# Optimization experiments

Hardware: AMD Instinct MI355X
Metric: run time of the kernel (lower is better)

Reference implementation:

```python
import jax, jax.numpy as jnp
import numpy as np

N_NODES = 100000
N_EDGES = 2000000
F_IN = 32
HID = 32
N_CLASS = 40


def _gru_cell(m, h, wih, whh, bih, bhh):
    # torch.nn.GRUCell math; wih/whh: [3H, H_in], gates ordered r, z, n
    gi = m @ wih.T + bih
    gh = h @ whh.T + bhh
    i_r, i_z, i_n = jnp.split(gi, 3, axis=-1)
    h_r, h_z, h_n = jnp.split(gh, 3, axis=-1)
    r = jax.nn.sigmoid(i_r + h_r)
    z = jax.nn.sigmoid(i_z + h_z)
    n = jnp.tanh(i_n + r * h_n)
    return (1.0 - z) * n + z * h


def _gated_conv(x, edge_index, edge_weight, w_proj, w_msg, wih, whh, bih, bhh):
    h = x @ w_proj                                   # [N, out]
    msg = (h @ w_msg)[edge_index[0]] * edge_weight[:, None]  # gather src -> [E, out]
    agg = jax.ops.segment_sum(msg, edge_index[1], num_segments=N_NODES)  # scatter-add to dst
    return _gru_cell(agg, h, wih, whh, bih, bhh)


def setup_inputs() -> dict:
    key = jax.random.key(0)
    ks = jax.random.split(key, 16)
    s = 0.1
    return {
        "x": jax.random.normal(ks[0], (N_NODES, F_IN), jnp.float32),
        "edge_index": jax.random.randint(ks[1], (2, N_EDGES), 0, N_NODES, jnp.int64),
        "edge_weight": jax.random.uniform(ks[2], (N_EDGES,), jnp.float32),
        "W1_proj": jax.random.normal(ks[3], (F_IN, HID), jnp.float32) * s,
        "W1_msg": jax.random.normal(ks[4], (HID, HID), jnp.float32) * s,
        "gru1_wih": jax.random.normal(ks[5], (3 * HID, HID), jnp.float32) * s,
        "gru1_whh": jax.random.normal(ks[6], (3 * HID, HID), jnp.float32) * s,
        "gru1_bih": jax.random.normal(ks[7], (3 * HID,), jnp.float32) * s,
        "gru1_bhh": jax.random.normal(ks[8], (3 * HID,), jnp.float32) * s,
        "W2_proj": jax.random.normal(ks[9], (HID, N_CLASS), jnp.float32) * s,
        "W2_msg": jax.random.normal(ks[10], (N_CLASS, N_CLASS), jnp.float32) * s,
        "gru2_wih": jax.random.normal(ks[11], (3 * N_CLASS, N_CLASS), jnp.float32) * s,
        "gru2_whh": jax.random.normal(ks[12], (3 * N_CLASS, N_CLASS), jnp.float32) * s,
        "gru2_bih": jax.random.normal(ks[13], (3 * N_CLASS,), jnp.float32) * s,
        "gru2_bhh": jax.random.normal(ks[14], (3 * N_CLASS,), jnp.float32) * s,
    }


def reference(x, edge_index, edge_weight, W1_proj, W1_msg, gru1_wih, gru1_whh,
              gru1_bih, gru1_bhh, W2_proj, W2_msg, gru2_wih, gru2_whh,
              gru2_bih, gru2_bhh):
    # eval mode: dropout is identity
    h = _gated_conv(x, edge_index, edge_weight, W1_proj, W1_msg,
                    gru1_wih, gru1_whh, gru1_bih, gru1_bhh)
    h = jax.nn.relu(h)
    h = _gated_conv(h, edge_index, edge_weight, W2_proj, W2_msg,
                    gru2_wih, gru2_whh, gru2_bih, gru2_bhh)
    return jax.nn.log_softmax(h, axis=-1)
```

## Files before the change

### kernel.cpp

```cpp
#include <hip/hip_runtime.h>
#include <math.h>

#define NN 100000
#define NP 100032
#define NE 2000000
#define FIN 32
#define H 32
#define NC 40

#define NBK 196
#define BSH 9
#define CAP 10880
#define EPT 16
#define EPB (256 * EPT)

typedef _Float16 half_t;
typedef __attribute__((ext_vector_type(8))) _Float16 half8;
typedef __attribute__((ext_vector_type(4))) _Float16 half4;
typedef __attribute__((ext_vector_type(4))) float f32x4;
typedef long long ll2 __attribute__((ext_vector_type(2)));

__device__ __forceinline__ float sigm_(float x) {
    return 1.0f / (1.0f + __expf(-x));
}
__device__ __forceinline__ float tanh_(float x) {
    x = fminf(fmaxf(x, -20.0f), 20.0f);
    float e = __expf(2.0f * x);
    return (e - 1.0f) / (e + 1.0f);
}

__global__ __launch_bounds__(256) void kA_bucket(const int* __restrict__ ei,
                                                 const float* __restrict__ ew,
                                                 int* __restrict__ gcur,
                                                 long long* __restrict__ rec) {
    __shared__ long long recs[EPB];
    __shared__ int gdst[EPB];
    __shared__ int cnt[NBK], base[NBK], sofs[NBK];
    __shared__ int ssc[256];
    int tid = threadIdx.x;
    for (int i = tid; i < NBK; i += 256) cnt[i] = 0;
    __syncthreads();
    int e0 = blockIdx.x * EPB;
    int dcache[EPT];
#pragma unroll
    for (int i = 0; i < EPT; ++i) {
        int e = e0 + i * 256 + tid;
        dcache[i] = (e < NE) ? ei[NE + e] : -1;
        if (e < NE) atomicAdd(&cnt[dcache[i] >> BSH], 1);
    }
    __syncthreads();
    int cv = (tid < NBK) ? cnt[tid] : 0;
    ssc[tid] = cv;
    __syncthreads();
    for (int off = 1; off < 256; off <<= 1) {
        int v = (tid >= off) ? ssc[tid - off] : 0;
        __syncthreads();
        ssc[tid] += v;
        __syncthreads();
    }
    if (tid < NBK) {
        sofs[tid] = ssc[tid] - cv;
        base[tid] = atomicAdd(&gcur[tid], cv);
        cnt[tid] = 0;
    }
    __syncthreads();
#pragma unroll
    for (int i = 0; i < EPT; ++i) {
        int e = e0 + i * 256 + tid;
        if (e < NE) {
            int d = dcache[i], s = ei[e];
            int b = d >> BSH;
            int r = atomicAdd(&cnt[b], 1);
            int slot = sofs[b] + r;
            int pos = base[b] + r;
            int lo = s | ((d & 511) << 17);
            recs[slot] = (long long)(unsigned)lo |
                         ((long long)__float_as_int(ew[e]) << 32);
            gdst[slot] = (pos < CAP) ? (b * CAP + pos) : -1;
        }
    }
    __syncthreads();
    int nrec = min(EPB, NE - e0);
    for (int i = tid; i < nrec; i += 256) {
        int gd = gdst[i];
        if (gd >= 0) rec[gd] = recs[i];
    }
}

__global__ __launch_bounds__(256) void kB_sort(const int* __restrict__ gcur,
                                               const int2* __restrict__ rec,
                                               int2* __restrict__ evs,
                                               int* __restrict__ ofs,
                                               int* __restrict__ ocn) {
    __shared__ int hist[2048], lofs[2048], ssc[256];
    int tid = threadIdx.x, b = blockIdx.x;
    int nb0 = b << BSH;
    int nnodes = min(512, NN - nb0);
    int cntb = min(gcur[b], CAP);
    for (int i = tid; i < 2048; i += 256) hist[i] = 0;
    __syncthreads();
    const int2* rb = rec + (size_t)b * CAP;
    for (int i = tid; i < cntb; i += 256) {
        int rx = rb[i].x;
        int bin = (((rx >> 17) & 511) << 2) | ((rx & 0x1FFFF) >> 15);
        atomicAdd(&hist[bin], 1);
    }
    __syncthreads();
    int base = tid * 8, ls = 0, lh[8];
#pragma unroll
    for (int j = 0; j < 8; ++j) {
        lh[j] = hist[base + j];
        ls += lh[j];
    }
    ssc[tid] = ls;
    __syncthreads();
    for (int off = 1; off < 256; off <<= 1) {
        int v = (tid >= off) ? ssc[tid - off] : 0;
        __syncthreads();
        ssc[tid] += v;
        __syncthreads();
    }
    int ex = ssc[tid] - ls;
#pragma unroll
    for (int j = 0; j < 8; ++j) {
        lofs[base + j] = ex;
        ex += lh[j];
    }
    __syncthreads();
    for (int l = tid; l < nnodes; l += 256) {
        int c = hist[4 * l] + hist[4 * l + 1] + hist[4 * l + 2] + hist[4 * l + 3];
        ofs[nb0 + l] = b * CAP + lofs[4 * l];
        ocn[nb0 + l] = c;
    }
    __syncthreads();
    for (int i = tid; i < 2048; i += 256) hist[i] = 0;
    __syncthreads();
    int2* eb = evs + (size_t)b * CAP;
    for (int i = tid; i < cntb; i += 256) {
        int2 r = rb[i];
        int bin = (((r.x >> 17) & 511) << 2) | ((r.x & 0x1FFFF) >> 15);
        int rk = atomicAdd(&hist[bin], 1);
        eb[lofs[bin] + rk] = make_int2(r.x & 0x1FFFF, r.y);
    }
}

__global__ __launch_bounds__(256) void k_wpre(const float* __restrict__ W2m,
                                              const float* __restrict__ wih2,
                                              float* __restrict__ M2,
                                              int* __restrict__ gcur) {
    int i = blockIdx.x * 256 + threadIdx.x;
    if (i < NBK) gcur[i] = 0;
    if (i >= NC * 3 * NC) return;
    int u = i / (3 * NC), col = i % (3 * NC);
    float acc = 0.f;
#pragma unroll
    for (int t = 0; t < NC; ++t) acc += W2m[u * NC + t] * wih2[col * NC + t];
    M2[i] = acc;
}

__global__ __launch_bounds__(256) void k_wc(const float* __restrict__ W1m,
                                            const float* __restrict__ wih1,
                                            const float* __restrict__ W2p,
                                            const float* __restrict__ M2,
                                            const float* __restrict__ whh1,
                                            const float* __restrict__ whh2,
                                            half_t* __restrict__ W1sw,
                                            half_t* __restrict__ W2sw) {
    int i = blockIdx.x * 256 + threadIdx.x;
    if (i < 8192) {
        int j = i & 7, lane = (i >> 3) & 63, ct = (i >> 9) & 7, s = i >> 12;
        int k = s * 32 + (lane >> 4) * 8 + j;
        int col = ct * 16 + (lane & 15);
        int g = col >> 5, jj = col & 31;
        float v = 0.f;
        if (g <= 2) {
            if (k < 32) {
                float acc = 0.f;
#pragma unroll
                for (int t = 0; t < H; ++t) acc += W1m[k * H + t] * wih1[(g * H + jj) * H + t];
                v = acc;
            } else if (g < 2) {
                v = whh1[(g * H + jj) * H + (k - 32)];
            }
        } else {
            if (k >= 32) v = whh1[(2 * H + jj) * H + (k - 32)];
        }
        W1sw[i] = (half_t)v;
    } else if (i < 8192 + 18432) {
        int i2 = i - 8192;
        int j = i2 & 7, lane = (i2 >> 3) & 63;
        int tt = i2 >> 9;
        int ct = tt % 12, s = tt / 12;
        int k = s * 32 + (lane >> 4) * 8 + j;
        int col = ct * 16 + (lane & 15);
        int g = col / 48, jj = col % 48;
        float v = 0.f;
        if (jj < NC) {
            if (g <= 2) {
                if (k < 32) {
                    float acc = 0.f;
#pragma unroll
                    for (int u = 0; u < NC; ++u)
                        acc += W2p[k * NC + u] * M2[u * 3 * NC + g * NC + jj];
                    v = acc;
                } else if (k < 72 && g < 2) {
                    v = whh2[(g * NC + jj) * NC + (k - 32)];
                }
            } else {
                if (k >= 32 && k < 72) v = whh2[(2 * NC + jj) * NC + (k - 32)];
            }
        }
        W2sw[i2] = (half_t)v;
    }
}

__global__ __launch_bounds__(256) void k1_proj(const float* __restrict__ x,
                                               const float* __restrict__ Wp,
                                               half_t* __restrict__ Xc1,
                                               half_t* __restrict__ Hd) {
    __shared__ float sWp[FIN * H];
    __shared__ float sx[8][FIN];
    int tid = threadIdx.x;
    for (int i = tid; i < FIN * H; i += 256) sWp[i] = Wp[i];
    int nb = blockIdx.x * 8;
    int nl = tid >> 5, j = tid & 31;
    int n = nb + nl;
    if (n < NN) sx[nl][j] = x[(size_t)n * FIN + j];
    __syncthreads();
    float acc = 0.f;
#pragma unroll
    for (int k = 0; k < FIN; ++k) acc += sx[nl][k] * sWp[k * H + j];
    if (n < NN) {
        half_t hv = (half_t)acc;
        Xc1[(size_t)n * 64 + 32 + j] = hv;
        Hd[(size_t)n * 32 + j] = hv;
    }
}

__global__ __launch_bounds__(320) void k4_proj2(const half_t* __restrict__ Hh,
                                                const float* __restrict__ Wp,
                                                half_t* __restrict__ Xc2) {
    __shared__ float sWp[FIN * NC];
    __shared__ float shn[8][FIN];
    int tid = threadIdx.x;
    for (int i = tid; i < FIN * NC; i += 320) sWp[i] = Wp[i];
    int nb = blockIdx.x * 8;
    if (tid < 256) {
        int r = tid >> 5, c = tid & 31;
        shn[r][c] = (float)Hh[(size_t)(nb + r) * 32 + c];
    }
    if (tid < 192) {
        int r = tid / 24, c = tid % 24;
        Xc2[(size_t)(nb + r) * 96 + 72 + c] = (half_t)0.f;
    }
    __syncthreads();
    int nl = tid / NC, j = tid % NC;
    int n = nb + nl;
    float acc = 0.f;
#pragma unroll
    for (int k = 0; k < FIN; ++k) acc += shn[nl][k] * sWp[k * NC + j];
    if (n < NN) Xc2[(size_t)n * 96 + 32 + j] = (half_t)acc;
}

template <int DSTR>
__global__ __launch_bounds__(256) void k_aggh(const int* __restrict__ ofs,
                                              const int* __restrict__ ocn,
                                              const int2* __restrict__ evs,
                                              const half_t* __restrict__ src,
                                              half_t* __restrict__ dst) {
    int idx = blockIdx.x * 256 + threadIdx.x;
    int n = idx >> 2, q = idx & 3;
    if (n >= NN) return;
    const half8* s8 = (const half8*)src + q;
    const long long* ev8 = (const long long*)evs;
    int e = ofs[n];
    int e1 = e + ocn[n];
    float acc[8] = {0.f, 0.f, 0.f, 0.f, 0.f, 0.f, 0.f, 0.f};
    if ((e & 1) && e < e1) {
        long long r = __builtin_nontemporal_load(ev8 + e);
        float w = __int_as_float((int)(r >> 32));
        half8 hv = s8[(size_t)(r & 0x1FFFF) * 4];
#pragma unroll
        for (int t = 0; t < 8; ++t) acc[t] += w * (float)hv[t];
        ++e;
    }
    for (; e + 8 <= e1; e += 8) {
        ll2 p0 = __builtin_nontemporal_load((const ll2*)(ev8 + e));
        ll2 p1 = __builtin_nontemporal_load((const ll2*)(ev8 + e + 2));
        ll2 p2 = __builtin_nontemporal_load((const ll2*)(ev8 + e + 4));
        ll2 p3 = __builtin_nontemporal_load((const ll2*)(ev8 + e + 6));
        half8 h0 = s8[(size_t)(p0[0] & 0x1FFFF) * 4];
        half8 h1 = s8[(size_t)(p0[1] & 0x1FFFF) * 4];
        half8 h2 = s8[(size_t)(p1[0] & 0x1FFFF) * 4];
        half8 h3 = s8[(size_t)(p1[1] & 0x1FFFF) * 4];
        half8 h4 = s8[(size_t)(p2[0] & 0x1FFFF) * 4];
        half8 h5 = s8[(size_t)(p2[1] & 0x1FFFF) * 4];
        half8 h6 = s8[(size_t)(p3[0] & 0x1FFFF) * 4];
        half8 h7 = s8[(size_t)(p3[1] & 0x1FFFF) * 4];
        float w0 = __int_as_float((int)(p0[0] >> 32));
        float w1 = __int_as_float((int)(p0[1] >> 32));
        float w2 = __int_as_float((int)(p1[0] >> 32));
        float w3 = __int_as_float((int)(p1[1] >> 32));
        float w4 = __int_as_float((int)(p2[0] >> 32));
        float w5 = __int_as_float((int)(p2[1] >> 32));
        float w6 = __int_as_float((int)(p3[0] >> 32));
        float w7 = __int_as_float((int)(p3[1] >> 32));
#pragma unroll
        for (int t = 0; t < 8; ++t) {
            acc[t] += w0 * (float)h0[t];
            acc[t] += w1 * (float)h1[t];
            acc[t] += w2 * (float)h2[t];
            acc[t] += w3 * (float)h3[t];
            acc[t] += w4 * (float)h4[t];
            acc[t] += w5 * (float)h5[t];
            acc[t] += w6 * (float)h6[t];
            acc[t] += w7 * (float)h7[t];
        }
    }
    if (e + 4 <= e1) {
        ll2 p0 = __builtin_nontemporal_load((const ll2*)(ev8 + e));
        ll2 p1 = __builtin_nontemporal_load((const ll2*)(ev8 + e + 2));
        half8 h0 = s8[(size_t)(p0[0] & 0x1FFFF) * 4];
        half8 h1 = s8[(size_t)(p0[1] & 0x1FFFF) * 4];
        half8 h2 = s8[(size_t)(p1[0] & 0x1FFFF) * 4];
        half8 h3 = s8[(size_t)(p1[1] & 0x1FFFF) * 4];
        float w0 = __int_as_float((int)(p0[0] >> 32));
        float w1 = __int_as_float((int)(p0[1] >> 32));
        float w2 = __int_as_float((int)(p1[0] >> 32));
        float w3 = __int_as_float((int)(p1[1] >> 32));
#pragma unroll
        for (int t = 0; t < 8; ++t) {
            acc[t] += w0 * (float)h0[t];
            acc[t] += w1 * (float)h1[t];
            acc[t] += w2 * (float)h2[t];
            acc[t] += w3 * (float)h3[t];
        }
        e += 4;
    }
    if (e + 2 <= e1) {
        ll2 p0 = __builtin_nontemporal_load((const ll2*)(ev8 + e));
        half8 h0 = s8[(size_t)(p0[0] & 0x1FFFF) * 4];
        half8 h1 = s8[(size_t)(p0[1] & 0x1FFFF) * 4];
        float w0 = __int_as_float((int)(p0[0] >> 32));
        float w1 = __int_as_float((int)(p0[1] >> 32));
#pragma unroll
        for (int t = 0; t < 8; ++t) {
            acc[t] += w0 * (float)h0[t];
            acc[t] += w1 * (float)h1[t];
        }
        e += 2;
    }
    if (e < e1) {
        long long r = __builtin_nontemporal_load(ev8 + e);
        float w = __int_as_float((int)(r >> 32));
        half8 hv = s8[(size_t)(r & 0x1FFFF) * 4];
#pragma unroll
        for (int t = 0; t < 8; ++t) acc[t] += w * (float)hv[t];
    }
    half8 o;
#pragma unroll
    for (int t = 0; t < 8; ++t) o[t] = (half_t)acc[t];
    *(half8*)(dst + (size_t)n * DSTR + q * 8) = o;
}

__global__ __launch_bounds__(256) void k3m(const half_t* __restrict__ Xc1,
                                           const half8* __restrict__ W1sw,
                                           const float* __restrict__ bih,
                                           const float* __restrict__ bhh,
                                           half_t* __restrict__ Hh) {
    int tid = threadIdx.x;
    int wave = tid >> 6, lane = tid & 63;
    int m16 = lane & 15, q = lane >> 4;
    int nb = blockIdx.x * 64 + wave * 16;
    const half8* xr = (const half8*)(Xc1 + (size_t)(nb + m16) * 64);
    half8 a0 = xr[q];
    half8 a1 = xr[4 + q];
    f32x4 acc[8];
#pragma unroll
    for (int ct = 0; ct < 8; ++ct) acc[ct] = (f32x4){0.f, 0.f, 0.f, 0.f};
#pragma unroll
    for (int ct = 0; ct < 8; ++ct) {
        acc[ct] = __builtin_amdgcn_mfma_f32_16x16x32_f16(a0, W1sw[ct * 64 + lane], acc[ct], 0, 0, 0);
        acc[ct] = __builtin_amdgcn_mfma_f32_16x16x32_f16(a1, W1sw[(8 + ct) * 64 + lane], acc[ct], 0, 0, 0);
    }
#pragma unroll
    for (int ct = 0; ct < 2; ++ct) {
        int j = ct * 16 + m16;
        float br = bih[j] + bhh[j];
        float bz = bih[H + j] + bhh[H + j];
        float bi = bih[2 * H + j], bh = bhh[2 * H + j];
#pragma unroll
        for (int m = 0; m < 4; ++m) {
            int node = nb + q * 4 + m;
            float r = sigm_(acc[ct][m] + br);
            float z = sigm_(acc[2 + ct][m] + bz);
            float ng = tanh_(acc[4 + ct][m] + bi + r * (acc[6 + ct][m] + bh));
            float hj = (float)Xc1[(size_t)node * 64 + 32 + j];
            float o = fmaxf((1.f - z) * ng + z * hj, 0.f);
            if (node < NN) Hh[(size_t)node * 32 + j] = (half_t)o;
        }
    }
}

__global__ __launch_bounds__(256) void k6m(const half_t* __restrict__ Xc2,
                                           const half8* __restrict__ W2sw,
                                           const float* __restrict__ bih,
                                           const float* __restrict__ bhh,
                                           float* __restrict__ out) {
    int tid = threadIdx.x;
    int wave = tid >> 6, lane = tid & 63;
    int m16 = lane & 15, q = lane >> 4;
    int nb = blockIdx.x * 64 + wave * 16;
    const half8* xr = (const half8*)(Xc2 + (size_t)(nb + m16) * 96);
    half8 a0 = xr[q], a1 = xr[4 + q], a2 = xr[8 + q];
    f32x4 acc[12];
#pragma unroll
    for (int ct = 0; ct < 12; ++ct) acc[ct] = (f32x4){0.f, 0.f, 0.f, 0.f};
#pragma unroll
    for (int ct = 0; ct < 12; ++ct) {
        acc[ct] = __builtin_amdgcn_mfma_f32_16x16x32_f16(a0, W2sw[ct * 64 + lane], acc[ct], 0, 0, 0);
        acc[ct] = __builtin_amdgcn_mfma_f32_16x16x32_f16(a1, W2sw[(12 + ct) * 64 + lane], acc[ct], 0, 0, 0);
        acc[ct] = __builtin_amdgcn_mfma_f32_16x16x32_f16(a2, W2sw[(24 + ct) * 64 + lane], acc[ct], 0, 0, 0);
    }
    float v[3][4];
#pragma unroll
    for (int ct = 0; ct < 3; ++ct) {
        int j = ct * 16 + m16;
        int jc = (j < NC) ? j : (NC - 1);
        float br = bih[jc] + bhh[jc];
        float bz = bih[NC + jc] + bhh[NC + jc];
        float bi = bih[2 * NC + jc], bh = bhh[2 * NC + jc];
#pragma unroll
        for (int m = 0; m < 4; ++m) {
            int node = nb + q * 4 + m;
            float r = sigm_(acc[ct][m] + br);
            float z = sigm_(acc[3 + ct][m] + bz);
            float ng = tanh_(acc[6 + ct][m] + bi + r * (acc[9 + ct][m] + bh));
            float hj = (float)Xc2[(size_t)node * 96 + 32 + jc];
            v[ct][m] = (1.f - z) * ng + z * hj;
        }
    }
    bool v2ok = (m16 < 8);
#pragma unroll
    for (int m = 0; m < 4; ++m) {
        float mx = fmaxf(v[0][m], v[1][m]);
        if (v2ok) mx = fmaxf(mx, v[2][m]);
#pragma unroll
        for (int d = 1; d < 16; d <<= 1) mx = fmaxf(mx, __shfl_xor(mx, d));
        float se = __expf(v[0][m] - mx) + __expf(v[1][m] - mx) +
                   (v2ok ? __expf(v[2][m] - mx) : 0.f);
#pragma unroll
        for (int d = 1; d < 16; d <<= 1) se += __shfl_xor(se, d);
        float ls = mx + __logf(se);
        int node = nb + q * 4 + m;
        if (node < NN) {
            out[(size_t)node * NC + m16] = v[0][m] - ls;
            out[(size_t)node * NC + 16 + m16] = v[1][m] - ls;
            if (v2ok) out[(size_t)node * NC + 32 + m16] = v[2][m] - ls;
        }
    }
}

extern "C" void kernel_launch(void* const* d_in, const int* in_sizes, int n_in,
                              void* d_out, int out_size, void* d_ws, size_t ws_size,
                              hipStream_t stream) {
    const float* x = (const float*)d_in[0];
    const int* ei = (const int*)d_in[1];
    const float* ew = (const float*)d_in[2];
    const float* W1p = (const float*)d_in[3];
    const float* W1m = (const float*)d_in[4];
    const float* g1wih = (const float*)d_in[5];
    const float* g1whh = (const float*)d_in[6];
    const float* g1bih = (const float*)d_in[7];
    const float* g1bhh = (const float*)d_in[8];
    const float* W2p = (const float*)d_in[9];
    const float* W2m = (const float*)d_in[10];
    const float* g2wih = (const float*)d_in[11];
    const float* g2whh = (const float*)d_in[12];
    const float* g2bih = (const float*)d_in[13];
    const float* g2bhh = (const float*)d_in[14];
    float* ws = (float*)d_ws;

    half_t* Xc = (half_t*)ws;
    half_t* Hd = (half_t*)(ws + 3201024);
    half_t* Hh = (half_t*)(ws + 4801536);
    int2* rec = (int2*)ws;
    int2* evs = (int2*)(ws + 6402048);
    int* ofs = (int*)(ws + 10667008);
    int* ocn = (int*)(ws + 10767008);
    int* gcur = (int*)(ws + 10867008);
    half_t* W1sw = (half_t*)(ws + 10867264);
    half_t* W2sw = W1sw + 8192;
    float* M2 = ws + 10880576;
    float* out = (float*)d_out;

    k_wpre<<<(NC * 3 * NC + 255) / 256, 256, 0, stream>>>(W2m, g2wih, M2, gcur);
    kA_bucket<<<(NE + EPB - 1) / EPB, 256, 0, stream>>>(ei, ew, gcur, (long long*)rec);
    kB_sort<<<NBK, 256, 0, stream>>>(gcur, rec, evs, ofs, ocn);
    k_wc<<<(8192 + 18432 + 255) / 256, 256, 0, stream>>>(
        W1m, g1wih, W2p, M2, g1whh, g2whh, W1sw, W2sw);

    k1_proj<<<NN / 8, 256, 0, stream>>>(x, W1p, Xc, Hd);
    k_aggh<64><<<(NN * 4 + 255) / 256, 256, 0, stream>>>(ofs, ocn, evs, Hd, Xc);
    k3m<<<NP / 64, 256, 0, stream>>>(Xc, (const half8*)W1sw, g1bih, g1bhh, Hh);

    k4_proj2<<<NN / 8, 320, 0, stream>>>(Hh, W2p, Xc);
    k_aggh<96><<<(NN * 4 + 255) / 256, 256, 0, stream>>>(ofs, ocn, evs, Hh, Xc);
    k6m<<<NP / 64, 256, 0, stream>>>(Xc, (const half8*)W2sw, g2bih, g2bhh, out);
}
```

Before: 303.7 us.

## Fuse aggregation, projection and GRU per layer into single kernels

```diff
diff --git a/kernel.cpp b/kernel.cpp
--- a/kernel.cpp
+++ b/kernel.cpp
@@ -14,9 +14,11 @@
 #define EPT 16
 #define EPB (256 * EPT)
 
+#define NPROJ 12500
+#define NWB 104
+
 typedef _Float16 half_t;
 typedef __attribute__((ext_vector_type(8))) _Float16 half8;
-typedef __attribute__((ext_vector_type(4))) _Float16 half4;
 typedef __attribute__((ext_vector_type(4))) float f32x4;
 typedef long long ll2 __attribute__((ext_vector_type(2)));
 
@@ -29,253 +31,16 @@
     return (e - 1.0f) / (e + 1.0f);
 }
 
-__global__ __launch_bounds__(256) void kA_bucket(const int* __restrict__ ei,
-                                                 const float* __restrict__ ew,
-                                                 int* __restrict__ gcur,
-                                                 long long* __restrict__ rec) {
-    __shared__ long long recs[EPB];
-    __shared__ int gdst[EPB];
-    __shared__ int cnt[NBK], base[NBK], sofs[NBK];
-    __shared__ int ssc[256];
-    int tid = threadIdx.x;
-    for (int i = tid; i < NBK; i += 256) cnt[i] = 0;
-    __syncthreads();
-    int e0 = blockIdx.x * EPB;
-    int dcache[EPT];
-#pragma unroll
-    for (int i = 0; i < EPT; ++i) {
-        int e = e0 + i * 256 + tid;
-        dcache[i] = (e < NE) ? ei[NE + e] : -1;
-        if (e < NE) atomicAdd(&cnt[dcache[i] >> BSH], 1);
-    }
-    __syncthreads();
-    int cv = (tid < NBK) ? cnt[tid] : 0;
-    ssc[tid] = cv;
-    __syncthreads();
-    for (int off = 1; off < 256; off <<= 1) {
-        int v = (tid >= off) ? ssc[tid - off] : 0;
-        __syncthreads();
-        ssc[tid] += v;
-        __syncthreads();
-    }
-    if (tid < NBK) {
-        sofs[tid] = ssc[tid] - cv;
-        base[tid] = atomicAdd(&gcur[tid], cv);
-        cnt[tid] = 0;
-    }
-    __syncthreads();
-#pragma unroll
-    for (int i = 0; i < EPT; ++i) {
-        int e = e0 + i * 256 + tid;
-        if (e < NE) {
-            int d = dcache[i], s = ei[e];
-            int b = d >> BSH;
-            int r = atomicAdd(&cnt[b], 1);
-            int slot = sofs[b] + r;
-            int pos = base[b] + r;
-            int lo = s | ((d & 511) << 17);
-            recs[slot] = (long long)(unsigned)lo |
-                         ((long long)__float_as_int(ew[e]) << 32);
-            gdst[slot] = (pos < CAP) ? (b * CAP + pos) : -1;
-        }
-    }
-    __syncthreads();
-    int nrec = min(EPB, NE - e0);
-    for (int i = tid; i < nrec; i += 256) {
-        int gd = gdst[i];
-        if (gd >= 0) rec[gd] = recs[i];
-    }
-}
-
-__global__ __launch_bounds__(256) void kB_sort(const int* __restrict__ gcur,
-                                               const int2* __restrict__ rec,
-                                               int2* __restrict__ evs,
-                                               int* __restrict__ ofs,
-                                               int* __restrict__ ocn) {
-    __shared__ int hist[2048], lofs[2048], ssc[256];
-    int tid = threadIdx.x, b = blockIdx.x;
-    int nb0 = b << BSH;
-    int nnodes = min(512, NN - nb0);
-    int cntb = min(gcur[b], CAP);
-    for (int i = tid; i < 2048; i += 256) hist[i] = 0;
-    __syncthreads();
-    const int2* rb = rec + (size_t)b * CAP;
-    for (int i = tid; i < cntb; i += 256) {
-        int rx = rb[i].x;
-        int bin = (((rx >> 17) & 511) << 2) | ((rx & 0x1FFFF) >> 15);
-        atomicAdd(&hist[bin], 1);
-    }
-    __syncthreads();
-    int base = tid * 8, ls = 0, lh[8];
-#pragma unroll
-    for (int j = 0; j < 8; ++j) {
-        lh[j] = hist[base + j];
-        ls += lh[j];
-    }
-    ssc[tid] = ls;
-    __syncthreads();
-    for (int off = 1; off < 256; off <<= 1) {
-        int v = (tid >= off) ? ssc[tid - off] : 0;
-        __syncthreads();
-        ssc[tid] += v;
-        __syncthreads();
-    }
-    int ex = ssc[tid] - ls;
-#pragma unroll
-    for (int j = 0; j < 8; ++j) {
-        lofs[base + j] = ex;
-        ex += lh[j];
-    }
-    __syncthreads();
-    for (int l = tid; l < nnodes; l += 256) {
-        int c = hist[4 * l] + hist[4 * l + 1] + hist[4 * l + 2] + hist[4 * l + 3];
-        ofs[nb0 + l] = b * CAP + lofs[4 * l];
-        ocn[nb0 + l] = c;
-    }
-    __syncthreads();
-    for (int i = tid; i < 2048; i += 256) hist[i] = 0;
-    __syncthreads();
-    int2* eb = evs + (size_t)b * CAP;
-    for (int i = tid; i < cntb; i += 256) {
-        int2 r = rb[i];
-        int bin = (((r.x >> 17) & 511) << 2) | ((r.x & 0x1FFFF) >> 15);
-        int rk = atomicAdd(&hist[bin], 1);
-        eb[lofs[bin] + rk] = make_int2(r.x & 0x1FFFF, r.y);
-    }
-}
-
-__global__ __launch_bounds__(256) void k_wpre(const float* __restrict__ W2m,
-                                              const float* __restrict__ wih2,
-                                              float* __restrict__ M2,
-                                              int* __restrict__ gcur) {
-    int i = blockIdx.x * 256 + threadIdx.x;
-    if (i < NBK) gcur[i] = 0;
-    if (i >= NC * 3 * NC) return;
-    int u = i / (3 * NC), col = i % (3 * NC);
-    float acc = 0.f;
-#pragma unroll
-    for (int t = 0; t < NC; ++t) acc += W2m[u * NC + t] * wih2[col * NC + t];
-    M2[i] = acc;
-}
-
-__global__ __launch_bounds__(256) void k_wc(const float* __restrict__ W1m,
-                                            const float* __restrict__ wih1,
-                                            const float* __restrict__ W2p,
-                                            const float* __restrict__ M2,
-                                            const float* __restrict__ whh1,
-                                            const float* __restrict__ whh2,
-                                            half_t* __restrict__ W1sw,
-                                            half_t* __restrict__ W2sw) {
-    int i = blockIdx.x * 256 + threadIdx.x;
-    if (i < 8192) {
-        int j = i & 7, lane = (i >> 3) & 63, ct = (i >> 9) & 7, s = i >> 12;
-        int k = s * 32 + (lane >> 4) * 8 + j;
-        int col = ct * 16 + (lane & 15);
-        int g = col >> 5, jj = col & 31;
-        float v = 0.f;
-        if (g <= 2) {
-            if (k < 32) {
-                float acc = 0.f;
-#pragma unroll
-                for (int t = 0; t < H; ++t) acc += W1m[k * H + t] * wih1[(g * H + jj) * H + t];
-                v = acc;
-            } else if (g < 2) {
-                v = whh1[(g * H + jj) * H + (k - 32)];
-            }
-        } else {
-            if (k >= 32) v = whh1[(2 * H + jj) * H + (k - 32)];
-        }
-        W1sw[i] = (half_t)v;
-    } else if (i < 8192 + 18432) {
-        int i2 = i - 8192;
-        int j = i2 & 7, lane = (i2 >> 3) & 63;
-        int tt = i2 >> 9;
-        int ct = tt % 12, s = tt / 12;
-        int k = s * 32 + (lane >> 4) * 8 + j;
-        int col = ct * 16 + (lane & 15);
-        int g = col / 48, jj = col % 48;
-        float v = 0.f;
-        if (jj < NC) {
-            if (g <= 2) {
-                if (k < 32) {
-                    float acc = 0.f;
-#pragma unroll
-                    for (int u = 0; u < NC; ++u)
-                        acc += W2p[k * NC + u] * M2[u * 3 * NC + g * NC + jj];
-                    v = acc;
-                } else if (k < 72 && g < 2) {
-                    v = whh2[(g * NC + jj) * NC + (k - 32)];
-                }
-            } else {
-                if (k >= 32 && k < 72) v = whh2[(2 * NC + jj) * NC + (k - 32)];
-            }
-        }
-        W2sw[i2] = (half_t)v;
-    }
-}
-
-__global__ __launch_bounds__(256) void k1_proj(const float* __restrict__ x,
-                                               const float* __restrict__ Wp,
-                                               half_t* __restrict__ Xc1,
-                                               half_t* __restrict__ Hd) {
-    __shared__ float sWp[FIN * H];
-    __shared__ float sx[8][FIN];
-    int tid = threadIdx.x;
-    for (int i = tid; i < FIN * H; i += 256) sWp[i] = Wp[i];
-    int nb = blockIdx.x * 8;
-    int nl = tid >> 5, j = tid & 31;
-    int n = nb + nl;
-    if (n < NN) sx[nl][j] = x[(size_t)n * FIN + j];
-    __syncthreads();
-    float acc = 0.f;
-#pragma unroll
-    for (int k = 0; k < FIN; ++k) acc += sx[nl][k] * sWp[k * H + j];
-    if (n < NN) {
-        half_t hv = (half_t)acc;
-        Xc1[(size_t)n * 64 + 32 + j] = hv;
-        Hd[(size_t)n * 32 + j] = hv;
-    }
-}
-
-__global__ __launch_bounds__(320) void k4_proj2(const half_t* __restrict__ Hh,
-                                                const float* __restrict__ Wp,
-                                                half_t* __restrict__ Xc2) {
-    __shared__ float sWp[FIN * NC];
-    __shared__ float shn[8][FIN];
-    int tid = threadIdx.x;
-    for (int i = tid; i < FIN * NC; i += 320) sWp[i] = Wp[i];
-    int nb = blockIdx.x * 8;
-    if (tid < 256) {
-        int r = tid >> 5, c = tid & 31;
-        shn[r][c] = (float)Hh[(size_t)(nb + r) * 32 + c];
-    }
-    if (tid < 192) {
-        int r = tid / 24, c = tid % 24;
-        Xc2[(size_t)(nb + r) * 96 + 72 + c] = (half_t)0.f;
-    }
-    __syncthreads();
-    int nl = tid / NC, j = tid % NC;
-    int n = nb + nl;
-    float acc = 0.f;
-#pragma unroll
-    for (int k = 0; k < FIN; ++k) acc += shn[nl][k] * sWp[k * NC + j];
-    if (n < NN) Xc2[(size_t)n * 96 + 32 + j] = (half_t)acc;
-}
-
-template <int DSTR>
-__global__ __launch_bounds__(256) void k_aggh(const int* __restrict__ ofs,
-                                              const int* __restrict__ ocn,
-                                              const int2* __restrict__ evs,
-                                              const half_t* __restrict__ src,
-                                              half_t* __restrict__ dst) {
-    int idx = blockIdx.x * 256 + threadIdx.x;
-    int n = idx >> 2, q = idx & 3;
-    if (n >= NN) return;
+__device__ __forceinline__ void agg_run(int n, int q,
+                                        const int* __restrict__ ofs,
+                                        const int* __restrict__ ocn,
+                                        const int2* __restrict__ evs,
+                                        const half_t* __restrict__ src,
+                                        float* acc) {
     const half8* s8 = (const half8*)src + q;
     const long long* ev8 = (const long long*)evs;
     int e = ofs[n];
     int e1 = e + ocn[n];
-    float acc[8] = {0.f, 0.f, 0.f, 0.f, 0.f, 0.f, 0.f, 0.f};
     if ((e & 1) && e < e1) {
         long long r = __builtin_nontemporal_load(ev8 + e);
         float w = __int_as_float((int)(r >> 32));
@@ -357,31 +122,247 @@
 #pragma unroll
         for (int t = 0; t < 8; ++t) acc[t] += w * (float)hv[t];
     }
+}
+
+__global__ __launch_bounds__(256) void kA_bucket(const int* __restrict__ ei,
+                                                 const float* __restrict__ ew,
+                                                 int* __restrict__ gcur,
+                                                 long long* __restrict__ rec) {
+    __shared__ long long recs[EPB];
+    __shared__ int gdst[EPB];
+    __shared__ int cnt[NBK], base[NBK], sofs[NBK];
+    __shared__ int ssc[256];
+    int tid = threadIdx.x;
+    for (int i = tid; i < NBK; i += 256) cnt[i] = 0;
+    __syncthreads();
+    int e0 = blockIdx.x * EPB;
+    int dcache[EPT];
+#pragma unroll
+    for (int i = 0; i < EPT; ++i) {
+        int e = e0 + i * 256 + tid;
+        dcache[i] = (e < NE) ? ei[NE + e] : -1;
+        if (e < NE) atomicAdd(&cnt[dcache[i] >> BSH], 1);
+    }
+    __syncthreads();
+    int cv = (tid < NBK) ? cnt[tid] : 0;
+    ssc[tid] = cv;
+    __syncthreads();
+    for (int off = 1; off < 256; off <<= 1) {
+        int v = (tid >= off) ? ssc[tid - off] : 0;
+        __syncthreads();
+        ssc[tid] += v;
+        __syncthreads();
+    }
+    if (tid < NBK) {
+        sofs[tid] = ssc[tid] - cv;
+        base[tid] = atomicAdd(&gcur[tid], cv);
+        cnt[tid] = 0;
+    }
+    __syncthreads();
+#pragma unroll
+    for (int i = 0; i < EPT; ++i) {
+        int e = e0 + i * 256 + tid;
+        if (e < NE) {
+            int d = dcache[i], s = ei[e];
+            int b = d >> BSH;
+            int r = atomicAdd(&cnt[b], 1);
+            int slot = sofs[b] + r;
+            int pos = base[b] + r;
+            int lo = s | ((d & 511) << 17);
+            recs[slot] = (long long)(unsigned)lo |
+                         ((long long)__float_as_int(ew[e]) << 32);
+            gdst[slot] = (pos < CAP) ? (b * CAP + pos) : -1;
+        }
+    }
+    __syncthreads();
+    int nrec = min(EPB, NE - e0);
+    for (int i = tid; i < nrec; i += 256) {
+        int gd = gdst[i];
+        if (gd >= 0) rec[gd] = recs[i];
+    }
+}
+
+__global__ __launch_bounds__(256) void kB_sort(const int* __restrict__ gcur,
+                                               const int2* __restrict__ rec,
+                                               int2* __restrict__ evs,
+                                               int* __restrict__ ofs,
+                                               int* __restrict__ ocn) {
+    __shared__ int hist[2048], lofs[2048], ssc[256];
+    int tid = threadIdx.x, b = blockIdx.x;
+    int nb0 = b << BSH;
+    int nnodes = min(512, NN - nb0);
+    int cntb = min(gcur[b], CAP);
+    for (int i = tid; i < 2048; i += 256) hist[i] = 0;
+    __syncthreads();
+    const int2* rb = rec + (size_t)b * CAP;
+    for (int i = tid; i < cntb; i += 256) {
+        int rx = rb[i].x;
+        int bin = (((rx >> 17) & 511) << 2) | ((rx & 0x1FFFF) >> 15);
+        atomicAdd(&hist[bin], 1);
+    }
+    __syncthreads();
+    int base = tid * 8, ls = 0, lh[8];
+#pragma unroll
+    for (int j = 0; j < 8; ++j) {
+        lh[j] = hist[base + j];
+        ls += lh[j];
+    }
+    ssc[tid] = ls;
+    __syncthreads();
+    for (int off = 1; off < 256; off <<= 1) {
+        int v = (tid >= off) ? ssc[tid - off] : 0;
+        __syncthreads();
+        ssc[tid] += v;
+        __syncthreads();
+    }
+    int ex = ssc[tid] - ls;
+#pragma unroll
+    for (int j = 0; j < 8; ++j) {
+        lofs[base + j] = ex;
+        ex += lh[j];
+    }
+    __syncthreads();
+    for (int l = tid; l < nnodes; l += 256) {
+        int c = hist[4 * l] + hist[4 * l + 1] + hist[4 * l + 2] + hist[4 * l + 3];
+        ofs[nb0 + l] = b * CAP + lofs[4 * l];
+        ocn[nb0 + l] = c;
+    }
+    __syncthreads();
+    for (int i = tid; i < 2048; i += 256) hist[i] = 0;
+    __syncthreads();
+    int2* eb = evs + (size_t)b * CAP;
+    for (int i = tid; i < cntb; i += 256) {
+        int2 r = rb[i];
+        int bin = (((r.x >> 17) & 511) << 2) | ((r.x & 0x1FFFF) >> 15);
+        int rk = atomicAdd(&hist[bin], 1);
+        eb[lofs[bin] + rk] = make_int2(r.x & 0x1FFFF, r.y);
+    }
+}
+
+__global__ __launch_bounds__(256) void k_prep(const float* __restrict__ x,
+                                              const float* __restrict__ W1p,
+                                              const float* __restrict__ W1m,
+                                              const float* __restrict__ wih1,
+                                              const float* __restrict__ whh1,
+                                              const float* __restrict__ W2p,
+                                              const float* __restrict__ W2m,
+                                              const float* __restrict__ wih2,
+                                              const float* __restrict__ whh2,
+                                              half_t* __restrict__ Hd,
+                                              half_t* __restrict__ W1sw,
+                                              half_t* __restrict__ W2sw,
+                                              int* __restrict__ gcur) {
+    __shared__ float sWp[FIN * H];
+    __shared__ float sx[8][FIN];
+    __shared__ float P2l[32 * NC];
+    int b = blockIdx.x, tid = threadIdx.x;
+    if (b < NPROJ) {
+        for (int i = tid; i < FIN * H; i += 256) sWp[i] = W1p[i];
+        int nb = b * 8;
+        int nl = tid >> 5, j = tid & 31;
+        int n = nb + nl;
+        if (n < NN) sx[nl][j] = x[(size_t)n * FIN + j];
+        __syncthreads();
+        float acc = 0.f;
+#pragma unroll
+        for (int k = 0; k < FIN; ++k) acc += sx[nl][k] * sWp[k * H + j];
+        if (n < NN) Hd[(size_t)n * 32 + j] = (half_t)acc;
+        return;
+    }
+    int wb = b - NPROJ;
+    if (wb == 0 && tid < NBK) gcur[tid] = 0;
+    int i = wb * 256 + tid;
+    if (i < 8192) {
+        int j = i & 7, lane = (i >> 3) & 63, ct = (i >> 9) & 7, s = i >> 12;
+        int k = s * 32 + (lane >> 4) * 8 + j;
+        int col = ct * 16 + (lane & 15);
+        int g = col >> 5, jj = col & 31;
+        float v = 0.f;
+        if (g <= 2) {
+            if (k < 32) {
+                float acc = 0.f;
+#pragma unroll
+                for (int t = 0; t < H; ++t) acc += W1m[k * H + t] * wih1[(g * H + jj) * H + t];
+                v = acc;
+            } else if (g < 2) {
+                v = whh1[(g * H + jj) * H + (k - 32)];
+            }
+        } else {
+            if (k >= 32) v = whh1[(2 * H + jj) * H + (k - 32)];
+        }
+        W1sw[i] = (half_t)v;
+    } else {
+        for (int e = tid; e < 32 * NC; e += 256) {
+            int k = e / NC, t = e % NC;
+            float a = 0.f;
+#pragma unroll
+            for (int u = 0; u < NC; ++u) a += W2p[k * NC + u] * W2m[u * NC + t];
+            P2l[e] = a;
+        }
+        __syncthreads();
+        int i2 = i - 8192;
+        int j = i2 & 7, lane = (i2 >> 3) & 63;
+        int tt = i2 >> 9;
+        int ct = tt % 12, s = tt / 12;
+        int k = s * 32 + (lane >> 4) * 8 + j;
+        int col = ct * 16 + (lane & 15);
+        int g = col / 48, jj = col % 48;
+        float v = 0.f;
+        if (jj < NC) {
+            if (g <= 2) {
+                if (k < 32) {
+                    float acc = 0.f;
+#pragma unroll
+                    for (int t = 0; t < NC; ++t)
+                        acc += P2l[k * NC + t] * wih2[(g * NC + jj) * NC + t];
+                    v = acc;
+                } else if (k < 72 && g < 2) {
+                    v = whh2[(g * NC + jj) * NC + (k - 32)];
+                }
+            } else {
+                if (k >= 32 && k < 72) v = whh2[(2 * NC + jj) * NC + (k - 32)];
+            }
+        }
+        W2sw[i2] = (half_t)v;
+    }
+}
+
+__global__ __launch_bounds__(256) void k_l1(const int* __restrict__ ofs,
+                                            const int* __restrict__ ocn,
+                                            const int2* __restrict__ evs,
+                                            const half_t* __restrict__ Hd,
+                                            const half8* __restrict__ W1sw,
+                                            const float* __restrict__ bih,
+                                            const float* __restrict__ bhh,
+                                            half_t* __restrict__ Hh) {
+    __shared__ half8 aggT[64][4];
+    __shared__ half8 hd8[64][4];
+    int tid = threadIdx.x;
+    int nl = tid >> 2, q = tid & 3;
+    int n = blockIdx.x * 64 + nl;
+    half8 hz;
+#pragma unroll
+    for (int t = 0; t < 8; ++t) hz[t] = (half_t)0.f;
+    hd8[nl][q] = (n < NN) ? ((const half8*)Hd)[(size_t)n * 4 + q] : hz;
+    float acc[8] = {0.f, 0.f, 0.f, 0.f, 0.f, 0.f, 0.f, 0.f};
+    if (n < NN) agg_run(n, q, ofs, ocn, evs, Hd, acc);
     half8 o;
 #pragma unroll
     for (int t = 0; t < 8; ++t) o[t] = (half_t)acc[t];
-    *(half8*)(dst + (size_t)n * DSTR + q * 8) = o;
-}
-
-__global__ __launch_bounds__(256) void k3m(const half_t* __restrict__ Xc1,
-                                           const half8* __restrict__ W1sw,
-                                           const float* __restrict__ bih,
-                                           const float* __restrict__ bhh,
-                                           half_t* __restrict__ Hh) {
-    int tid = threadIdx.x;
+    aggT[nl][q] = o;
+    __syncthreads();
     int wave = tid >> 6, lane = tid & 63;
-    int m16 = lane & 15, q = lane >> 4;
-    int nb = blockIdx.x * 64 + wave * 16;
-    const half8* xr = (const half8*)(Xc1 + (size_t)(nb + m16) * 64);
-    half8 a0 = xr[q];
-    half8 a1 = xr[4 + q];
-    f32x4 acc[8];
-#pragma unroll
-    for (int ct = 0; ct < 8; ++ct) acc[ct] = (f32x4){0.f, 0.f, 0.f, 0.f};
+    int m16 = lane & 15, qq = lane >> 4;
+    int nbw = blockIdx.x * 64 + wave * 16;
+    half8 a0 = aggT[wave * 16 + m16][qq];
+    half8 a1 = hd8[wave * 16 + m16][qq];
+    f32x4 macc[8];
+#pragma unroll
+    for (int ct = 0; ct < 8; ++ct) macc[ct] = (f32x4){0.f, 0.f, 0.f, 0.f};
 #pragma unroll
     for (int ct = 0; ct < 8; ++ct) {
-        acc[ct] = __builtin_amdgcn_mfma_f32_16x16x32_f16(a0, W1sw[ct * 64 + lane], acc[ct], 0, 0, 0);
-        acc[ct] = __builtin_amdgcn_mfma_f32_16x16x32_f16(a1, W1sw[(8 + ct) * 64 + lane], acc[ct], 0, 0, 0);
+        macc[ct] = __builtin_amdgcn_mfma_f32_16x16x32_f16(a0, W1sw[ct * 64 + lane], macc[ct], 0, 0, 0);
+        macc[ct] = __builtin_amdgcn_mfma_f32_16x16x32_f16(a1, W1sw[(8 + ct) * 64 + lane], macc[ct], 0, 0, 0);
     }
 #pragma unroll
     for (int ct = 0; ct < 2; ++ct) {
@@ -391,36 +372,79 @@
         float bi = bih[2 * H + j], bh = bhh[2 * H + j];
 #pragma unroll
         for (int m = 0; m < 4; ++m) {
-            int node = nb + q * 4 + m;
-            float r = sigm_(acc[ct][m] + br);
-            float z = sigm_(acc[2 + ct][m] + bz);
-            float ng = tanh_(acc[4 + ct][m] + bi + r * (acc[6 + ct][m] + bh));
-            float hj = (float)Xc1[(size_t)node * 64 + 32 + j];
-            float o = fmaxf((1.f - z) * ng + z * hj, 0.f);
-            if (node < NN) Hh[(size_t)node * 32 + j] = (half_t)o;
-        }
-    }
-}
-
-__global__ __launch_bounds__(256) void k6m(const half_t* __restrict__ Xc2,
-                                           const half8* __restrict__ W2sw,
-                                           const float* __restrict__ bih,
-                                           const float* __restrict__ bhh,
-                                           float* __restrict__ out) {
+            int node = nbw + qq * 4 + m;
+            float r = sigm_(macc[ct][m] + br);
+            float z = sigm_(macc[2 + ct][m] + bz);
+            float ng = tanh_(macc[4 + ct][m] + bi + r * (macc[6 + ct][m] + bh));
+            float hj = (float)hd8[wave * 16 + qq * 4 + m][j >> 3][j & 7];
+            float out = fmaxf((1.f - z) * ng + z * hj, 0.f);
+            if (node < NN) Hh[(size_t)node * 32 + j] = (half_t)out;
+        }
+    }
+}
+
+__global__ __launch_bounds__(256) void k_l2(const int* __restrict__ ofs,
+                                            const int* __restrict__ ocn,
+                                            const int2* __restrict__ evs,
+                                            const half_t* __restrict__ Hh,
+                                            const half8* __restrict__ W2sw,
+                                            const float* __restrict__ W2p,
+                                            const float* __restrict__ bih,
+                                            const float* __restrict__ bhh,
+                                            float* __restrict__ out) {
+    __shared__ half8 aggT[64][4];
+    __shared__ half8 hh8[64][4];
+    __shared__ half8 h2c8[64][8];
+    __shared__ float sW[FIN * NC];
     int tid = threadIdx.x;
+    int nl = tid >> 2, q = tid & 3;
+    int n = blockIdx.x * 64 + nl;
+    for (int i = tid; i < FIN * NC; i += 256) sW[i] = W2p[i];
+    half8 hz;
+#pragma unroll
+    for (int t = 0; t < 8; ++t) hz[t] = (half_t)0.f;
+    hh8[nl][q] = (n < NN) ? ((const half8*)Hh)[(size_t)n * 4 + q] : hz;
+    float acc[8] = {0.f, 0.f, 0.f, 0.f, 0.f, 0.f, 0.f, 0.f};
+    if (n < NN) agg_run(n, q, ofs, ocn, evs, Hh, acc);
+    half8 o;
+#pragma unroll
+    for (int t = 0; t < 8; ++t) o[t] = (half_t)acc[t];
+    aggT[nl][q] = o;
+    __syncthreads();
+    {
+        half8 hr[4];
+#pragma unroll
+        for (int t = 0; t < 4; ++t) hr[t] = hh8[nl][t];
+        half_t* h2row = (half_t*)h2c8[nl];
+        float a[10];
+#pragma unroll
+        for (int j0 = 0; j0 < 10; ++j0) a[j0] = 0.f;
+#pragma unroll
+        for (int k = 0; k < FIN; ++k) {
+            float hk = (float)hr[k >> 3][k & 7];
+#pragma unroll
+            for (int j0 = 0; j0 < 10; ++j0) a[j0] += hk * sW[k * NC + q * 10 + j0];
+        }
+#pragma unroll
+        for (int j0 = 0; j0 < 10; ++j0) h2row[q * 10 + j0] = (half_t)a[j0];
+#pragma unroll
+        for (int j0 = 0; j0 < 6; ++j0) h2row[40 + q * 6 + j0] = (half_t)0.f;
+    }
+    __syncthreads();
     int wave = tid >> 6, lane = tid & 63;
-    int m16 = lane & 15, q = lane >> 4;
-    int nb = blockIdx.x * 64 + wave * 16;
-    const half8* xr = (const half8*)(Xc2 + (size_t)(nb + m16) * 96);
-    half8 a0 = xr[q], a1 = xr[4 + q], a2 = xr[8 + q];
-    f32x4 acc[12];
-#pragma unroll
-    for (int ct = 0; ct < 12; ++ct) acc[ct] = (f32x4){0.f, 0.f, 0.f, 0.f};
+    int m16 = lane & 15, qq = lane >> 4;
+    int nbw = blockIdx.x * 64 + wave * 16;
+    half8 a0 = aggT[wave * 16 + m16][qq];
+    half8 a1 = h2c8[wave * 16 + m16][qq];
+    half8 a2 = h2c8[wave * 16 + m16][4 + qq];
+    f32x4 macc[12];
+#pragma unroll
+    for (int ct = 0; ct < 12; ++ct) macc[ct] = (f32x4){0.f, 0.f, 0.f, 0.f};
 #pragma unroll
     for (int ct = 0; ct < 12; ++ct) {
-        acc[ct] = __builtin_amdgcn_mfma_f32_16x16x32_f16(a0, W2sw[ct * 64 + lane], acc[ct], 0, 0, 0);
-        acc[ct] = __builtin_amdgcn_mfma_f32_16x16x32_f16(a1, W2sw[(12 + ct) * 64 + lane], acc[ct], 0, 0, 0);
-        acc[ct] = __builtin_amdgcn_mfma_f32_16x16x32_f16(a2, W2sw[(24 + ct) * 64 + lane], acc[ct], 0, 0, 0);
+        macc[ct] = __builtin_amdgcn_mfma_f32_16x16x32_f16(a0, W2sw[ct * 64 + lane], macc[ct], 0, 0, 0);
+        macc[ct] = __builtin_amdgcn_mfma_f32_16x16x32_f16(a1, W2sw[(12 + ct) * 64 + lane], macc[ct], 0, 0, 0);
+        macc[ct] = __builtin_amdgcn_mfma_f32_16x16x32_f16(a2, W2sw[(24 + ct) * 64 + lane], macc[ct], 0, 0, 0);
     }
     float v[3][4];
 #pragma unroll
@@ -432,11 +456,10 @@
         float bi = bih[2 * NC + jc], bh = bhh[2 * NC + jc];
 #pragma unroll
         for (int m = 0; m < 4; ++m) {
-            int node = nb + q * 4 + m;
-            float r = sigm_(acc[ct][m] + br);
-            float z = sigm_(acc[3 + ct][m] + bz);
-            float ng = tanh_(acc[6 + ct][m] + bi + r * (acc[9 + ct][m] + bh));
-            float hj = (float)Xc2[(size_t)node * 96 + 32 + jc];
+            float r = sigm_(macc[ct][m] + br);
+            float z = sigm_(macc[3 + ct][m] + bz);
+            float ng = tanh_(macc[6 + ct][m] + bi + r * (macc[9 + ct][m] + bh));
+            float hj = (float)((const half_t*)h2c8[wave * 16 + qq * 4 + m])[jc];
             v[ct][m] = (1.f - z) * ng + z * hj;
         }
     }
@@ -452,7 +475,7 @@
 #pragma unroll
         for (int d = 1; d < 16; d <<= 1) se += __shfl_xor(se, d);
         float ls = mx + __logf(se);
-        int node = nb + q * 4 + m;
+        int node = nbw + qq * 4 + m;
         if (node < NN) {
             out[(size_t)node * NC + m16] = v[0][m] - ls;
             out[(size_t)node * NC + 16 + m16] = v[1][m] - ls;
@@ -481,30 +504,24 @@
     const float* g2bhh = (const float*)d_in[14];
     float* ws = (float*)d_ws;
 
-    half_t* Xc = (half_t*)ws;
-    half_t* Hd = (half_t*)(ws + 3201024);
-    half_t* Hh = (half_t*)(ws + 4801536);
-    int2* rec = (int2*)ws;
-    int2* evs = (int2*)(ws + 6402048);
-    int* ofs = (int*)(ws + 10667008);
-    int* ocn = (int*)(ws + 10767008);
-    int* gcur = (int*)(ws + 10867008);
-    half_t* W1sw = (half_t*)(ws + 10867264);
+    long long* rec = (long long*)ws;
+    int2* evs = (int2*)(ws + 4264960);
+    half_t* Hd = (half_t*)(ws + 8529920);
+    half_t* Hh = (half_t*)(ws + 10130176);
+    int* ofs = (int*)(ws + 11730432);
+    int* ocn = (int*)(ws + 11830432);
+    int* gcur = (int*)(ws + 11930432);
+    half_t* W1sw = (half_t*)(ws + 11930688);
     half_t* W2sw = W1sw + 8192;
-    float* M2 = ws + 10880576;
     float* out = (float*)d_out;
 
-    k_wpre<<<(NC * 3 * NC + 255) / 256, 256, 0, stream>>>(W2m, g2wih, M2, gcur);
-    kA_bucket<<<(NE + EPB - 1) / EPB, 256, 0, stream>>>(ei, ew, gcur, (long long*)rec);
-    kB_sort<<<NBK, 256, 0, stream>>>(gcur, rec, evs, ofs, ocn);
-    k_wc<<<(8192 + 18432 + 255) / 256, 256, 0, stream>>>(
-        W1m, g1wih, W2p, M2, g1whh, g2whh, W1sw, W2sw);
-
-    k1_proj<<<NN / 8, 256, 0, stream>>>(x, W1p, Xc, Hd);
-    k_aggh<64><<<(NN * 4 + 255) / 256, 256, 0, stream>>>(ofs, ocn, evs, Hd, Xc);
-    k3m<<<NP / 64, 256, 0, stream>>>(Xc, (const half8*)W1sw, g1bih, g1bhh, Hh);
-
-    k4_proj2<<<NN / 8, 320, 0, stream>>>(Hh, W2p, Xc);
-    k_aggh<96><<<(NN * 4 + 255) / 256, 256, 0, stream>>>(ofs, ocn, evs, Hh, Xc);
-    k6m<<<NP / 64, 256, 0, stream>>>(Xc, (const half8*)W2sw, g2bih, g2bhh, out);
-}
+    k_prep<<<NPROJ + NWB, 256, 0, stream>>>(x, W1p, W1m, g1wih, g1whh,
+                                            W2p, W2m, g2wih, g2whh,
+                                            Hd, W1sw, W2sw, gcur);
+    kA_bucket<<<(NE + EPB - 1) / EPB, 256, 0, stream>>>(ei, ew, gcur, rec);
+    kB_sort<<<NBK, 256, 0, stream>>>(gcur, (const int2*)rec, evs, ofs, ocn);
+    k_l1<<<NP / 64, 256, 0, stream>>>(ofs, ocn, evs, Hd, (const half8*)W1sw,
+                                      g1bih, g1bhh, Hh);
+    k_l2<<<NP / 64, 256, 0, stream>>>(ofs, ocn, evs, Hh, (const half8*)W2sw,
+                                      W2p, g2bih, g2bhh, out);
+}
```

Result: faster. 278.4 us (-8.3%).
